# Performance work log

Measured on AMD Instinct MI355X. Metric: run time of the kernel, lower is better.

Reference implementation:

```python
import jax, jax.numpy as jnp
import numpy as np
from jax import lax

N, T, IN, H, HEADS, OUT, E = 20000, 32, 32, 64, 4, 1, 320000


def setup_inputs() -> dict:
    key = jax.random.key(0)
    ks = jax.random.split(key, 18)
    s = 0.1
    inp = {
        "x": jax.random.normal(ks[0], (N, T, IN), jnp.float32),
        "edge_index": jax.random.randint(ks[1], (2, E), 0, N, dtype=jnp.int32),
        # LSTM layer 0 (PyTorch gate order i,f,g,o)
        "l0_Wih": jax.random.normal(ks[2], (4 * H, IN), jnp.float32) * s,
        "l0_Whh": jax.random.normal(ks[3], (4 * H, H), jnp.float32) * s,
        "l0_bih": jax.random.normal(ks[4], (4 * H,), jnp.float32) * s,
        "l0_bhh": jax.random.normal(ks[5], (4 * H,), jnp.float32) * s,
        # LSTM layer 1
        "l1_Wih": jax.random.normal(ks[6], (4 * H, H), jnp.float32) * s,
        "l1_Whh": jax.random.normal(ks[7], (4 * H, H), jnp.float32) * s,
        "l1_bih": jax.random.normal(ks[8], (4 * H,), jnp.float32) * s,
        "l1_bhh": jax.random.normal(ks[9], (4 * H,), jnp.float32) * s,
        # GAT layer 1: in=H, out=H, heads=HEADS (concat)
        "g1_w": jax.random.normal(ks[10], (H, HEADS * H), jnp.float32) * s,
        "g1_as": jax.random.normal(ks[11], (1, HEADS, H), jnp.float32) * s,
        "g1_ad": jax.random.normal(ks[12], (1, HEADS, H), jnp.float32) * s,
        "g1_b": jnp.zeros((HEADS * H,), jnp.float32),
        # GAT layer 2: in=HEADS*H, out=OUT, heads=1
        "g2_w": jax.random.normal(ks[13], (HEADS * H, OUT), jnp.float32) * s,
        "g2_as": jax.random.normal(ks[14], (1, 1, OUT), jnp.float32) * s,
        "g2_ad": jax.random.normal(ks[15], (1, 1, OUT), jnp.float32) * s,
        "g2_b": jnp.zeros((OUT,), jnp.float32),
    }
    return inp


def _lstm_layer(x, Wih, Whh, bih, bhh):
    # x: [N, T, F] -> [N, T, H]
    n = x.shape[0]
    h0 = jnp.zeros((n, Whh.shape[1]), x.dtype)

    def step(carry, xt):
        h, c = carry
        g = xt @ Wih.T + h @ Whh.T + bih + bhh  # [N, 4H]
        i, f, gg, o = jnp.split(g, 4, axis=-1)
        c = jax.nn.sigmoid(f) * c + jax.nn.sigmoid(i) * jnp.tanh(gg)
        h = jax.nn.sigmoid(o) * jnp.tanh(c)
        return (h, c), h

    _, hs = lax.scan(step, (h0, h0), jnp.swapaxes(x, 0, 1))
    return jnp.swapaxes(hs, 0, 1)


def _gat(x, src, dst, n, W, a_src, a_dst, b, heads, outc):
    # PyG GATConv (eval mode, add_self_loops already applied to src/dst)
    xh = (x @ W).reshape(n, heads, outc)              # [N, heads, C]
    al_s = (xh * a_src).sum(-1)                       # [N, heads]
    al_d = (xh * a_dst).sum(-1)
    e = jax.nn.leaky_relu(al_s[src] + al_d[dst], 0.2)  # [E, heads]
    m = jax.ops.segment_max(e, dst, num_segments=n)
    m = jnp.where(jnp.isfinite(m), m, 0.0)
    ex = jnp.exp(e - m[dst])
    den = jax.ops.segment_sum(ex, dst, num_segments=n)
    w = ex / (den[dst] + 1e-16)                       # segment softmax over dst
    out = jax.ops.segment_sum(xh[src] * w[..., None], dst, num_segments=n)
    return out.reshape(n, heads * outc) + b


def reference(x, edge_index, l0_Wih, l0_Whh, l0_bih, l0_bhh, l1_Wih, l1_Whh,
              l1_bih, l1_bhh, g1_w, g1_as, g1_ad, g1_b, g2_w, g2_as, g2_ad, g2_b):
    n = x.shape[0]
    loops = jnp.arange(n, dtype=edge_index.dtype)
    ei = jnp.concatenate([edge_index, jnp.stack([loops, loops])], axis=1)
    src, dst = ei[0], ei[1]
    h = _lstm_layer(x, l0_Wih, l0_Whh, l0_bih, l0_bhh)
    h = _lstm_layer(h, l1_Wih, l1_Whh, l1_bih, l1_bhh)
    h = h[:, -1, :]  # node features from last timestep
    h = jax.nn.relu(_gat(h, src, dst, n, g1_w, g1_as, g1_ad, g1_b, HEADS, H))
    return _gat(h, src, dst, n, g2_w, g2_as, g2_ad, g2_b, 1, OUT)
```

## Files before the change

kernel.cpp:

```cpp
#include <hip/hip_runtime.h>
#include <math.h>

#define NN   20000
#define TT   32
#define INF_ 32
#define HID  64
#define NH   4
#define EE   320000
#define ETOT (EE + NN)
#define ZROW 164
#define NB   80

typedef __attribute__((ext_vector_type(8))) short bf16x8;
typedef __attribute__((ext_vector_type(4))) short short4v;
typedef __attribute__((ext_vector_type(4))) float f32x4;

static __device__ __forceinline__ float lrelu(float x){ return x>0.0f ? x : 0.2f*x; }

static __device__ __forceinline__ unsigned short f2bf(float f){
  unsigned u = __float_as_uint(f);
  unsigned r = u + 0x7fffu + ((u>>16)&1u);
  return (unsigned short)(r>>16);
}
static __device__ __forceinline__ float bf2f(unsigned short h){ return __uint_as_float(((unsigned)h)<<16); }

static __device__ __forceinline__ float lstm_cell(float gi, float gf, float gg, float go, float& c){
  float ef = __expf(-gf), ei = __expf(-gi), eg = __expf(-2.0f*gg);
  float pN = c*(1.0f+ei)*(1.0f+eg) + (1.0f-eg)*(1.0f+ef);
  float pD = (1.0f+ef)*(1.0f+ei)*(1.0f+eg);
  float cc = pN * __builtin_amdgcn_rcpf(pD);
  c = cc;
  float eo = __expf(-go), ec = __expf(-2.0f*cc);
  return (1.0f-ec) * __builtin_amdgcn_rcpf((1.0f+eo)*(1.0f+ec));
}

static __device__ __forceinline__ void edge_sd(const int* __restrict__ ei, int e, int& s, int& d){
  if (e < EE){ s = ei[e]; d = ei[EE + e]; } else { s = e - EE; d = s; }
}

__global__ void kzero_int(int* __restrict__ p, int n){
  int i = blockIdx.x*256 + threadIdx.x;
  if (i < n) p[i] = 0;
}

__global__ void pack_weights(const float* __restrict__ Wih0, const float* __restrict__ Whh0,
                             const float* __restrict__ bih0, const float* __restrict__ bhh0,
                             const float* __restrict__ Wih1, const float* __restrict__ Whh1,
                             const float* __restrict__ bih1, const float* __restrict__ bhh1,
                             unsigned short* __restrict__ Wpk,
                             float* __restrict__ b0, float* __restrict__ b1){
  int idx = blockIdx.x*256 + threadIdx.x;
  if (idx < 49152){
    int fb = idx >> 9;
    int h  = fb & 1;
    int t2 = fb >> 1;
    int ks = t2 % 3, T2 = t2 / 3;
    int T  = T2 & 1, w = T2 >> 1;
    int r  = idx & 511;
    int l  = r >> 3, j = r & 7;
    int pr = l & 15;
    int g  = (pr&3)*64 + w*8 + T*4 + (pr>>2);
    int k  = ks*32 + 4*(l>>4) + (j & 3) + 16*(j >> 2);
    float src = (k < 32) ? Wih0[g*32 + k] : Whh0[g*64 + (k - 32)];
    unsigned short hi = f2bf(src);
    Wpk[idx] = h ? f2bf(src - bf2f(hi)) : hi;
  } else if (idx < 114688){
    int idx2 = idx - 49152;
    int fb = idx2 >> 9;
    int h  = fb & 1;
    int t2 = fb >> 1;
    int ks = t2 & 3, T2 = t2 >> 2;
    int T  = T2 & 1, w = T2 >> 1;
    int r  = idx2 & 511;
    int l  = r >> 3, j = r & 7;
    int pr = l & 15;
    int g  = (pr&3)*64 + w*8 + T*4 + (pr>>2);
    int k  = ks*32 + 4*(l>>4) + (j & 3) + 16*(j >> 2);
    float src = (k < 64) ? Wih1[g*64 + k] : Whh1[g*64 + (k - 64)];
    unsigned short hi = f2bf(src);
    Wpk[idx] = h ? f2bf(src - bf2f(hi)) : hi;
  } else {
    int m = idx - 114688;
    if (m < 256) b0[m] = bih0[m] + bhh0[m];
    else if (m < 512) b1[m-256] = bih1[m-256] + bhh1[m-256];
  }
}

__global__ void count_deg(const int* __restrict__ ei, int* __restrict__ deg){
  int e = blockIdx.x*256 + threadIdx.x;
  if (e >= ETOT) return;
  int s, d; edge_sd(ei, e, s, d);
  atomicAdd(deg + d, 1);
}

__global__ void scan_deg(const int* __restrict__ deg, int* __restrict__ indptr, int* __restrict__ cursor){
  __shared__ int part[256];
  const int t = threadIdx.x;
  const int CH = (NN + 255) / 256;
  const int c0 = t * CH;
  int sum = 0;
  for (int i=0;i<CH;i++){ int idx=c0+i; if (idx<NN) sum += deg[idx]; }
  part[t] = sum; __syncthreads();
  int val = sum;
  for (int off=1; off<256; off<<=1){
    int add = (t>=off) ? part[t-off] : 0;
    __syncthreads();
    val += add; part[t] = val;
    __syncthreads();
  }
  int run = val - sum;
  for (int i=0;i<CH;i++){
    int idx=c0+i;
    if (idx<NN){ indptr[idx]=run; cursor[idx]=run; run += deg[idx]; }
  }
  if (t == 0) indptr[NN] = ETOT;
}

__global__ void scatter_edges(const int* __restrict__ ei, int* __restrict__ cursor, int* __restrict__ csr_src){
  int e = blockIdx.x*256 + threadIdx.x;
  if (e >= ETOT) return;
  int s, d; edge_sd(ei, e, s, d);
  int pos = atomicAdd(cursor + d, 1);
  csr_src[pos] = s;
}

#define PIN_LOAD(dst, p) asm volatile( \
    "global_load_dwordx4 %0, %1, off\n\t" \
    "s_waitcnt vmcnt(0)" \
    : "=&v"(dst) : "v"(p))

__global__ __launch_bounds__(512, 2)
__attribute__((amdgpu_waves_per_eu(2, 2)))
void lstm_mfma(
    const float* __restrict__ x,
    const unsigned short* __restrict__ Wpk,
    const float* __restrict__ b0, const float* __restrict__ b1,
    float* __restrict__ h1out)
{
  __shared__ unsigned short Zh[NB*ZROW];
  __shared__ unsigned short Zl[NB*ZROW];

  const int tid  = threadIdx.x;
  const int lane = tid & 63;
  const int w    = __builtin_amdgcn_readfirstlane(tid >> 6);
  const int ln15 = lane & 15;
  const int lq   = lane >> 4;
  const int gbase = blockIdx.x * NB;

  const bf16x8* wp = (const bf16x8*)Wpk;

  bf16x8 wA0h[2][3], wA0l[2][3], wA1h[2][4], wA1l[2][4];
#pragma unroll
  for (int T=0; T<2; ++T){
#pragma unroll
    for (int ks=0; ks<3; ++ks){
      PIN_LOAD(wA0h[T][ks], wp + (((w*2+T)*3+ks)*2+0)*64 + lane);
      PIN_LOAD(wA0l[T][ks], wp + (((w*2+T)*3+ks)*2+1)*64 + lane);
    }
#pragma unroll
    for (int ks=0; ks<4; ++ks){
      PIN_LOAD(wA1h[T][ks], wp + 6144 + (((w*2+T)*4+ks)*2+0)*64 + lane);
      PIN_LOAD(wA1l[T][ks], wp + 6144 + (((w*2+T)*4+ks)*2+1)*64 + lane);
    }
  }

  f32x4 bv0[2], bv1[2];
#pragma unroll
  for (int T=0; T<2; ++T){
    const int u = w*8 + T*4 + lq;
#pragma unroll
    for (int j=0; j<4; ++j){ bv0[T][j] = b0[j*64+u]; bv1[T][j] = b1[j*64+u]; }
  }

  const int xn1 = tid >> 3,        xk1 = (tid & 7)*4;
  const int xn2 = (512+tid) >> 3,  xk2 = ((512+tid) & 7)*4;
  const float* xp1 = x + (size_t)(gbase + xn1)*(TT*INF_) + xk1;
  const float* xp2 = x + (size_t)(gbase + xn2)*(TT*INF_) + xk2;
  const bool x2 = (tid < 128);

  for (int i = tid; i < NB*ZROW/2; i += 512){ ((unsigned*)Zh)[i] = 0; ((unsigned*)Zl)[i] = 0; }
  __syncthreads();
  {
    float4 v = *(const float4*)xp1;
    unsigned short h_[4], l_[4];
    h_[0]=f2bf(v.x); h_[1]=f2bf(v.y); h_[2]=f2bf(v.z); h_[3]=f2bf(v.w);
    l_[0]=f2bf(v.x-bf2f(h_[0])); l_[1]=f2bf(v.y-bf2f(h_[1]));
    l_[2]=f2bf(v.z-bf2f(h_[2])); l_[3]=f2bf(v.w-bf2f(h_[3]));
    *(uint2*)&Zh[xn1*ZROW + xk1] = make_uint2((unsigned)h_[0]|((unsigned)h_[1]<<16),(unsigned)h_[2]|((unsigned)h_[3]<<16));
    *(uint2*)&Zl[xn1*ZROW + xk1] = make_uint2((unsigned)l_[0]|((unsigned)l_[1]<<16),(unsigned)l_[2]|((unsigned)l_[3]<<16));
    if (x2){
      float4 u = *(const float4*)xp2;
      h_[0]=f2bf(u.x); h_[1]=f2bf(u.y); h_[2]=f2bf(u.z); h_[3]=f2bf(u.w);
      l_[0]=f2bf(u.x-bf2f(h_[0])); l_[1]=f2bf(u.y-bf2f(h_[1]));
      l_[2]=f2bf(u.z-bf2f(h_[2])); l_[3]=f2bf(u.w-bf2f(h_[3]));
      *(uint2*)&Zh[xn2*ZROW + xk2] = make_uint2((unsigned)h_[0]|((unsigned)h_[1]<<16),(unsigned)h_[2]|((unsigned)h_[3]<<16));
      *(uint2*)&Zl[xn2*ZROW + xk2] = make_uint2((unsigned)l_[0]|((unsigned)l_[1]<<16),(unsigned)l_[2]|((unsigned)l_[3]<<16));
    }
  }
  __syncthreads();

  float c0[10], c1[10];
#pragma unroll
  for (int i=0;i<10;i++){ c0[i]=0.f; c1[i]=0.f; }
  f32x4 aL1[2][5];

#define ZFRAG(Zb, node, kz) ({                                            \
    const unsigned short* _p = &Zb[(node)*ZROW + (kz) + 4*lq];            \
    short4v _a = *(const short4v*)_p;                                     \
    short4v _b = *(const short4v*)(_p + 16);                              \
    __builtin_shufflevector(_a, _b, 0,1,2,3,4,5,6,7); })

#define MF(acc, A, B) acc = __builtin_amdgcn_mfma_f32_16x16x32_bf16((A),(B),(acc),0,0,0)

#define HWRITE(hv, col) {                                                 \
    const unsigned short _hh = f2bf(hv);                                  \
    Zh[_n*ZROW + (col)] = _hh;                                            \
    Zl[_n*ZROW + (col)] = f2bf((hv) - bf2f(_hh)); }

  for (int t=0; t<TT; ++t){
    float4 xv1, xv2;
    const bool dox = (t+1 < TT);
    if (dox){ xv1 = *(const float4*)(xp1 + (size_t)(t+1)*INF_);
              if (x2) xv2 = *(const float4*)(xp2 + (size_t)(t+1)*INF_); }

    if (t > 0){
#pragma unroll
      for (int T=0; T<2; ++T){
        const int uc = 96 + w*8 + T*4 + lq;
#pragma unroll
        for (int GG=0; GG<5; ++GG){
          const int _n = GG*16 + ln15;
          float h = lstm_cell(aL1[T][GG][0], aL1[T][GG][1], aL1[T][GG][2], aL1[T][GG][3], c1[T*5+GG]);
          HWRITE(h, uc);
        }
      }
    }

    f32x4 aL0[2][5];
#pragma unroll
    for (int T=0; T<2; ++T)
#pragma unroll
      for (int GG=0; GG<5; ++GG) aL0[T][GG] = bv0[T];

#pragma unroll
    for (int ks=0; ks<3; ++ks){
      const int kz = ks*32;
#pragma unroll
      for (int GG=0; GG<5; ++GG){
        const bf16x8 zh = ZFRAG(Zh, GG*16+ln15, kz);
        const bf16x8 zl = ZFRAG(Zl, GG*16+ln15, kz);
        MF(aL0[0][GG], wA0h[0][ks], zh); MF(aL0[0][GG], wA0h[0][ks], zl); MF(aL0[0][GG], wA0l[0][ks], zh);
        MF(aL0[1][GG], wA0h[1][ks], zh); MF(aL0[1][GG], wA0h[1][ks], zl); MF(aL0[1][GG], wA0l[1][ks], zh);
      }
    }
    __syncthreads();

#pragma unroll
    for (int T=0; T<2; ++T){
      const int uc = 32 + w*8 + T*4 + lq;
#pragma unroll
      for (int GG=0; GG<5; ++GG){
        const int _n = GG*16 + ln15;
        float h = lstm_cell(aL0[T][GG][0], aL0[T][GG][1], aL0[T][GG][2], aL0[T][GG][3], c0[T*5+GG]);
        HWRITE(h, uc);
      }
    }
    if (dox){
      unsigned short h_[4], l_[4];
      h_[0]=f2bf(xv1.x); h_[1]=f2bf(xv1.y); h_[2]=f2bf(xv1.z); h_[3]=f2bf(xv1.w);
      l_[0]=f2bf(xv1.x-bf2f(h_[0])); l_[1]=f2bf(xv1.y-bf2f(h_[1]));
      l_[2]=f2bf(xv1.z-bf2f(h_[2])); l_[3]=f2bf(xv1.w-bf2f(h_[3]));
      *(uint2*)&Zh[xn1*ZROW + xk1] = make_uint2((unsigned)h_[0]|((unsigned)h_[1]<<16),(unsigned)h_[2]|((unsigned)h_[3]<<16));
      *(uint2*)&Zl[xn1*ZROW + xk1] = make_uint2((unsigned)l_[0]|((unsigned)l_[1]<<16),(unsigned)l_[2]|((unsigned)l_[3]<<16));
      if (x2){
        h_[0]=f2bf(xv2.x); h_[1]=f2bf(xv2.y); h_[2]=f2bf(xv2.z); h_[3]=f2bf(xv2.w);
        l_[0]=f2bf(xv2.x-bf2f(h_[0])); l_[1]=f2bf(xv2.y-bf2f(h_[1]));
        l_[2]=f2bf(xv2.z-bf2f(h_[2])); l_[3]=f2bf(xv2.w-bf2f(h_[3]));
        *(uint2*)&Zh[xn2*ZROW + xk2] = make_uint2((unsigned)h_[0]|((unsigned)h_[1]<<16),(unsigned)h_[2]|((unsigned)h_[3]<<16));
        *(uint2*)&Zl[xn2*ZROW + xk2] = make_uint2((unsigned)l_[0]|((unsigned)l_[1]<<16),(unsigned)l_[2]|((unsigned)l_[3]<<16));
      }
    }

#pragma unroll
    for (int T=0; T<2; ++T)
#pragma unroll
      for (int GG=0; GG<5; ++GG) aL1[T][GG] = bv1[T];

#pragma unroll
    for (int ks=2; ks<4; ++ks){
      const int kz = 32 + ks*32;
#pragma unroll
      for (int GG=0; GG<5; ++GG){
        const bf16x8 zh = ZFRAG(Zh, GG*16+ln15, kz);
        const bf16x8 zl = ZFRAG(Zl, GG*16+ln15, kz);
        MF(aL1[0][GG], wA1h[0][ks], zh); MF(aL1[0][GG], wA1h[0][ks], zl); MF(aL1[0][GG], wA1l[0][ks], zh);
        MF(aL1[1][GG], wA1h[1][ks], zh); MF(aL1[1][GG], wA1h[1][ks], zl); MF(aL1[1][GG], wA1l[1][ks], zh);
      }
    }
    __syncthreads();

#pragma unroll
    for (int ks=0; ks<2; ++ks){
      const int kz = 32 + ks*32;
#pragma unroll
      for (int GG=0; GG<5; ++GG){
        const bf16x8 zh = ZFRAG(Zh, GG*16+ln15, kz);
        const bf16x8 zl = ZFRAG(Zl, GG*16+ln15, kz);
        MF(aL1[0][GG], wA1h[0][ks], zh); MF(aL1[0][GG], wA1h[0][ks], zl); MF(aL1[0][GG], wA1l[0][ks], zh);
        MF(aL1[1][GG], wA1h[1][ks], zh); MF(aL1[1][GG], wA1h[1][ks], zl); MF(aL1[1][GG], wA1l[1][ks], zh);
      }
    }
    __syncthreads();
  }

#pragma unroll
  for (int T=0; T<2; ++T){
    const int uc = 96 + w*8 + T*4 + lq;
#pragma unroll
    for (int GG=0; GG<5; ++GG){
      const int _n = GG*16 + ln15;
      float h = lstm_cell(aL1[T][GG][0], aL1[T][GG][1], aL1[T][GG][2], aL1[T][GG][3], c1[T*5+GG]);
      HWRITE(h, uc);
    }
  }
  __syncthreads();

  for (int o = tid; o < NB*64; o += 512){
    const int n = o >> 6, u = o & 63;
    h1out[(size_t)(gbase+n)*64 + u] = bf2f(Zh[n*ZROW + 96 + u]) + bf2f(Zl[n*ZROW + 96 + u]);
  }
#undef ZFRAG
#undef MF
#undef HWRITE
}

__global__ __launch_bounds__(256) void gat1_prep(const float* __restrict__ h1, const float* __restrict__ W,
  const float* __restrict__ as_, const float* __restrict__ ad_,
  float* __restrict__ xh, float* __restrict__ als, float* __restrict__ ald)
{
  __shared__ float hs[8][64];
  const int nb0 = blockIdx.x * 8;
  const int o  = threadIdx.x;
  const int q  = o >> 6, u = o & 63;
  for (int i = o; i < 512; i += 256){
    hs[i>>6][i&63] = h1[(size_t)(nb0 + (i>>6))*64 + (i&63)];
  }
  __syncthreads();
  float acc[8];
#pragma unroll
  for (int nd=0; nd<8; ++nd) acc[nd] = 0.f;
  for (int k=0; k<64; ++k){
    const float wv = W[k*256 + o];
#pragma unroll
    for (int nd=0; nd<8; ++nd) acc[nd] = fmaf(hs[nd][k], wv, acc[nd]);
  }
  const float asv = as_[o], adv = ad_[o];
#pragma unroll
  for (int nd=0; nd<8; ++nd){
    xh[(size_t)(nb0+nd)*256 + o] = acc[nd];
    float ps = acc[nd] * asv;
    float pd = acc[nd] * adv;
#pragma unroll
    for (int off=32; off>=1; off>>=1){ ps += __shfl_xor(ps, off); pd += __shfl_xor(pd, off); }
    if (u == 0){ als[(nb0+nd)*4 + q] = ps; ald[(nb0+nd)*4 + q] = pd; }
  }
}

__global__ __launch_bounds__(256) void gat1_gather(
  const int* __restrict__ indptr, const int* __restrict__ csr_src,
  const float* __restrict__ als, const float* __restrict__ ald,
  const float* __restrict__ xh,  const float* __restrict__ b1g,
  const float* __restrict__ w2,  const float* __restrict__ as2, const float* __restrict__ ad2,
  float* __restrict__ xh2, float* __restrict__ a2s, float* __restrict__ a2d)
{
  const int d = blockIdx.x*4 + (threadIdx.x >> 6);
  const int lane = threadIdx.x & 63;
  if (d >= NN) return;
  const int p0 = indptr[d], p1 = indptr[d+1];

  float aldv[4];
#pragma unroll
  for (int q=0;q<4;q++) aldv[q] = ald[d*4+q];

  float mx[4];
#pragma unroll
  for (int q=0;q<4;q++) mx[q] = -3.4e38f;
  for (int e=p0+lane; e<p1; e+=64){
    int s = csr_src[e];
#pragma unroll
    for (int q=0;q<4;q++){
      float ev = lrelu(als[s*4+q] + aldv[q]);
      mx[q] = fmaxf(mx[q], ev);
    }
  }
#pragma unroll
  for (int off=32; off>=1; off>>=1){
#pragma unroll
    for (int q=0;q<4;q++) mx[q] = fmaxf(mx[q], __shfl_xor(mx[q], off));
  }

  const int q = lane >> 4;
  const float mq = mx[q];
  const float aldq = aldv[q];
  float ax=0.f, ay=0.f, az=0.f, aw=0.f, den=0.f;
  int s_next = (p0 < p1) ? csr_src[p0] : 0;
  for (int e=p0; e<p1; ++e){
    const int s = s_next;
    if (e+1 < p1) s_next = csr_src[e+1];
    float ev = lrelu(als[s*4+q] + aldq);
    float ex = __expf(ev - mq);
    den += ex;
    float4 v = *(const float4*)(xh + (size_t)s*256 + lane*4);
    ax = fmaf(ex, v.x, ax); ay = fmaf(ex, v.y, ay);
    az = fmaf(ex, v.z, az); aw = fmaf(ex, v.w, aw);
  }
  const float rr = 1.0f/(den + 1e-16f);
  const int o = lane*4;
  float v0 = ax*rr + b1g[o+0];
  float v1 = ay*rr + b1g[o+1];
  float v2 = az*rr + b1g[o+2];
  float v3 = aw*rr + b1g[o+3];
  v0 = v0>0.f?v0:0.f; v1 = v1>0.f?v1:0.f; v2 = v2>0.f?v2:0.f; v3 = v3>0.f?v3:0.f;
  float part = v0*w2[o+0] + v1*w2[o+1] + v2*w2[o+2] + v3*w2[o+3];
#pragma unroll
  for (int off=32; off>=1; off>>=1) part += __shfl_xor(part, off);
  if (lane == 0){
    xh2[d] = part;
    a2s[d] = part * as2[0];
    a2d[d] = part * ad2[0];
  }
}

__global__ __launch_bounds__(256) void gat2_gather(
  const int* __restrict__ indptr, const int* __restrict__ csr_src,
  const float* __restrict__ a2s, const float* __restrict__ a2d,
  const float* __restrict__ xh2, const float* __restrict__ b2,
  float* __restrict__ out)
{
  const int d = blockIdx.x*4 + (threadIdx.x >> 6);
  const int lane = threadIdx.x & 63;
  if (d >= NN) return;
  const int p0 = indptr[d], p1 = indptr[d+1];
  const float add = a2d[d];

  float mx = -3.4e38f;
  for (int e=p0+lane; e<p1; e+=64){
    int s = csr_src[e];
    mx = fmaxf(mx, lrelu(a2s[s] + add));
  }
#pragma unroll
  for (int off=32; off>=1; off>>=1) mx = fmaxf(mx, __shfl_xor(mx, off));

  float den = 0.f, num = 0.f;
  for (int e=p0+lane; e<p1; e+=64){
    int s = csr_src[e];
    float ev = lrelu(a2s[s] + add);
    float ex = __expf(ev - mx);
    den += ex;
    num = fmaf(ex, xh2[s], num);
  }
#pragma unroll
  for (int off=32; off>=1; off>>=1){ den += __shfl_xor(den, off); num += __shfl_xor(num, off); }
  if (lane == 0) out[d] = num/(den + 1e-16f) + b2[0];
}

extern "C" void kernel_launch(void* const* d_in, const int* in_sizes, int n_in,
                              void* d_out, int out_size, void* d_ws, size_t ws_size,
                              hipStream_t stream)
{
  const float* x    = (const float*)d_in[0];
  const int*   ei   = (const int*)d_in[1];
  const float* Wih0 = (const float*)d_in[2];
  const float* Whh0 = (const float*)d_in[3];
  const float* bih0 = (const float*)d_in[4];
  const float* bhh0 = (const float*)d_in[5];
  const float* Wih1 = (const float*)d_in[6];
  const float* Whh1 = (const float*)d_in[7];
  const float* bih1 = (const float*)d_in[8];
  const float* bhh1 = (const float*)d_in[9];
  const float* g1w  = (const float*)d_in[10];
  const float* g1as = (const float*)d_in[11];
  const float* g1ad = (const float*)d_in[12];
  const float* g1b  = (const float*)d_in[13];
  const float* g2w  = (const float*)d_in[14];
  const float* g2as = (const float*)d_in[15];
  const float* g2ad = (const float*)d_in[16];
  const float* g2b  = (const float*)d_in[17];

  float* ws  = (float*)d_ws;
  unsigned short* Wpk = (unsigned short*)ws;
  float* b0  = ws + 57344;
  float* b1  = b0 + 256;
  float* h1  = b1 + 256;
  float* xh  = h1 + 1280000;
  float* als = xh + 5120000;
  float* ald = als + 80000;
  float* xh2 = ald + 80000;
  float* a2s = xh2 + 20000;
  float* a2d = a2s + 20000;
  int*   deg    = (int*)(a2d + 20000);
  int*   indptr = deg + 20000;
  int*   cursor = indptr + 20001;
  int*   csr    = cursor + 20000;

  kzero_int<<<(NN+255)/256, 256, 0, stream>>>(deg, NN);
  pack_weights<<<450, 256, 0, stream>>>(Wih0,Whh0,bih0,bhh0,Wih1,Whh1,bih1,bhh1,Wpk,b0,b1);
  count_deg<<<(ETOT+255)/256, 256, 0, stream>>>(ei, deg);
  scan_deg<<<1, 256, 0, stream>>>(deg, indptr, cursor);
  scatter_edges<<<(ETOT+255)/256, 256, 0, stream>>>(ei, cursor, csr);
  lstm_mfma<<<250, 512, 0, stream>>>(x, Wpk, b0, b1, h1);
  gat1_prep<<<NN/8, 256, 0, stream>>>(h1, g1w, g1as, g1ad, xh, als, ald);
  gat1_gather<<<(NN+3)/4, 256, 0, stream>>>(indptr, csr, als, ald, xh, g1b, g2w, g2as, g2ad, xh2, a2s, a2d);
  gat2_gather<<<(NN+3)/4, 256, 0, stream>>>(indptr, csr, a2s, a2d, xh2, g2b, (float*)d_out);
}
```

Before: 421.0 us.

## Split LSTM hidden tiles across 16 waves per block instead of 8

The LSTM kernel now launches 1024 threads per block, and each wave owns one 4-unit gate tile instead of two. Weight fragments, accumulators and cell state per thread are halved, and the weight packing is reindexed to match. This doubles the waves available to hide MFMA and LDS latency within each of the 250 blocks, since the grid underfills the CUs. The cost is heavier __syncthreads among 16 waves and more redundant LDS reads of the shared Z fragments per block.

```diff
diff --git a/kernel.cpp b/kernel.cpp
--- a/kernel.cpp
+++ b/kernel.cpp
@@ -54,12 +54,11 @@
     int fb = idx >> 9;
     int h  = fb & 1;
     int t2 = fb >> 1;
-    int ks = t2 % 3, T2 = t2 / 3;
-    int T  = T2 & 1, w = T2 >> 1;
+    int ks = t2 % 3, tl = t2 / 3;
     int r  = idx & 511;
     int l  = r >> 3, j = r & 7;
     int pr = l & 15;
-    int g  = (pr&3)*64 + w*8 + T*4 + (pr>>2);
+    int g  = (pr&3)*64 + tl*4 + (pr>>2);
     int k  = ks*32 + 4*(l>>4) + (j & 3) + 16*(j >> 2);
     float src = (k < 32) ? Wih0[g*32 + k] : Whh0[g*64 + (k - 32)];
     unsigned short hi = f2bf(src);
@@ -69,12 +68,11 @@
     int fb = idx2 >> 9;
     int h  = fb & 1;
     int t2 = fb >> 1;
-    int ks = t2 & 3, T2 = t2 >> 2;
-    int T  = T2 & 1, w = T2 >> 1;
+    int ks = t2 & 3, tl = t2 >> 2;
     int r  = idx2 & 511;
     int l  = r >> 3, j = r & 7;
     int pr = l & 15;
-    int g  = (pr&3)*64 + w*8 + T*4 + (pr>>2);
+    int g  = (pr&3)*64 + tl*4 + (pr>>2);
     int k  = ks*32 + 4*(l>>4) + (j & 3) + 16*(j >> 2);
     float src = (k < 64) ? Wih1[g*64 + k] : Whh1[g*64 + (k - 64)];
     unsigned short hi = f2bf(src);
@@ -129,8 +127,8 @@
     "s_waitcnt vmcnt(0)" \
     : "=&v"(dst) : "v"(p))
 
-__global__ __launch_bounds__(512, 2)
-__attribute__((amdgpu_waves_per_eu(2, 2)))
+__global__ __launch_bounds__(1024)
+__attribute__((amdgpu_waves_per_eu(4, 4)))
 void lstm_mfma(
     const float* __restrict__ x,
     const unsigned short* __restrict__ Wpk,
@@ -149,60 +147,47 @@
 
   const bf16x8* wp = (const bf16x8*)Wpk;
 
-  bf16x8 wA0h[2][3], wA0l[2][3], wA1h[2][4], wA1l[2][4];
-#pragma unroll
-  for (int T=0; T<2; ++T){
-#pragma unroll
-    for (int ks=0; ks<3; ++ks){
-      PIN_LOAD(wA0h[T][ks], wp + (((w*2+T)*3+ks)*2+0)*64 + lane);
-      PIN_LOAD(wA0l[T][ks], wp + (((w*2+T)*3+ks)*2+1)*64 + lane);
-    }
-#pragma unroll
-    for (int ks=0; ks<4; ++ks){
-      PIN_LOAD(wA1h[T][ks], wp + 6144 + (((w*2+T)*4+ks)*2+0)*64 + lane);
-      PIN_LOAD(wA1l[T][ks], wp + 6144 + (((w*2+T)*4+ks)*2+1)*64 + lane);
-    }
-  }
-
-  f32x4 bv0[2], bv1[2];
-#pragma unroll
-  for (int T=0; T<2; ++T){
-    const int u = w*8 + T*4 + lq;
-#pragma unroll
-    for (int j=0; j<4; ++j){ bv0[T][j] = b0[j*64+u]; bv1[T][j] = b1[j*64+u]; }
-  }
-
-  const int xn1 = tid >> 3,        xk1 = (tid & 7)*4;
-  const int xn2 = (512+tid) >> 3,  xk2 = ((512+tid) & 7)*4;
-  const float* xp1 = x + (size_t)(gbase + xn1)*(TT*INF_) + xk1;
-  const float* xp2 = x + (size_t)(gbase + xn2)*(TT*INF_) + xk2;
-  const bool x2 = (tid < 128);
-
-  for (int i = tid; i < NB*ZROW/2; i += 512){ ((unsigned*)Zh)[i] = 0; ((unsigned*)Zl)[i] = 0; }
+  bf16x8 wA0h[3], wA0l[3], wA1h[4], wA1l[4];
+#pragma unroll
+  for (int ks=0; ks<3; ++ks){
+    PIN_LOAD(wA0h[ks], wp + ((w*3+ks)*2+0)*64 + lane);
+    PIN_LOAD(wA0l[ks], wp + ((w*3+ks)*2+1)*64 + lane);
+  }
+#pragma unroll
+  for (int ks=0; ks<4; ++ks){
+    PIN_LOAD(wA1h[ks], wp + 6144 + ((w*4+ks)*2+0)*64 + lane);
+    PIN_LOAD(wA1l[ks], wp + 6144 + ((w*4+ks)*2+1)*64 + lane);
+  }
+
+  f32x4 bv0, bv1;
+  {
+    const int u = w*4 + lq;
+#pragma unroll
+    for (int j=0; j<4; ++j){ bv0[j] = b0[j*64+u]; bv1[j] = b1[j*64+u]; }
+  }
+
+  const int xn = tid >> 3;
+  const int xk = (tid & 7) * 4;
+  const float* xp = x + (size_t)(gbase + ((xn < NB) ? xn : 0))*(TT*INF_) + xk;
+  const bool xth = (tid < 640);
+
+  for (int i = tid; i < NB*ZROW/2; i += 1024){ ((unsigned*)Zh)[i] = 0; ((unsigned*)Zl)[i] = 0; }
   __syncthreads();
-  {
-    float4 v = *(const float4*)xp1;
+  if (xth){
+    float4 v = *(const float4*)xp;
     unsigned short h_[4], l_[4];
     h_[0]=f2bf(v.x); h_[1]=f2bf(v.y); h_[2]=f2bf(v.z); h_[3]=f2bf(v.w);
     l_[0]=f2bf(v.x-bf2f(h_[0])); l_[1]=f2bf(v.y-bf2f(h_[1]));
     l_[2]=f2bf(v.z-bf2f(h_[2])); l_[3]=f2bf(v.w-bf2f(h_[3]));
-    *(uint2*)&Zh[xn1*ZROW + xk1] = make_uint2((unsigned)h_[0]|((unsigned)h_[1]<<16),(unsigned)h_[2]|((unsigned)h_[3]<<16));
-    *(uint2*)&Zl[xn1*ZROW + xk1] = make_uint2((unsigned)l_[0]|((unsigned)l_[1]<<16),(unsigned)l_[2]|((unsigned)l_[3]<<16));
-    if (x2){
-      float4 u = *(const float4*)xp2;
-      h_[0]=f2bf(u.x); h_[1]=f2bf(u.y); h_[2]=f2bf(u.z); h_[3]=f2bf(u.w);
-      l_[0]=f2bf(u.x-bf2f(h_[0])); l_[1]=f2bf(u.y-bf2f(h_[1]));
-      l_[2]=f2bf(u.z-bf2f(h_[2])); l_[3]=f2bf(u.w-bf2f(h_[3]));
-      *(uint2*)&Zh[xn2*ZROW + xk2] = make_uint2((unsigned)h_[0]|((unsigned)h_[1]<<16),(unsigned)h_[2]|((unsigned)h_[3]<<16));
-      *(uint2*)&Zl[xn2*ZROW + xk2] = make_uint2((unsigned)l_[0]|((unsigned)l_[1]<<16),(unsigned)l_[2]|((unsigned)l_[3]<<16));
-    }
+    *(uint2*)&Zh[xn*ZROW + xk] = make_uint2((unsigned)h_[0]|((unsigned)h_[1]<<16),(unsigned)h_[2]|((unsigned)h_[3]<<16));
+    *(uint2*)&Zl[xn*ZROW + xk] = make_uint2((unsigned)l_[0]|((unsigned)l_[1]<<16),(unsigned)l_[2]|((unsigned)l_[3]<<16));
   }
   __syncthreads();
 
-  float c0[10], c1[10];
-#pragma unroll
-  for (int i=0;i<10;i++){ c0[i]=0.f; c1[i]=0.f; }
-  f32x4 aL1[2][5];
+  float c0[5], c1[5];
+#pragma unroll
+  for (int i=0;i<5;i++){ c0[i]=0.f; c1[i]=0.f; }
+  f32x4 aL1[5];
 
 #define ZFRAG(Zb, node, kz) ({                                            \
     const unsigned short* _p = &Zb[(node)*ZROW + (kz) + 4*lq];            \
@@ -218,29 +203,23 @@
     Zl[_n*ZROW + (col)] = f2bf((hv) - bf2f(_hh)); }
 
   for (int t=0; t<TT; ++t){
-    float4 xv1, xv2;
-    const bool dox = (t+1 < TT);
-    if (dox){ xv1 = *(const float4*)(xp1 + (size_t)(t+1)*INF_);
-              if (x2) xv2 = *(const float4*)(xp2 + (size_t)(t+1)*INF_); }
+    float4 xv;
+    const bool dox = xth && (t+1 < TT);
+    if (dox) xv = *(const float4*)(xp + (size_t)(t+1)*INF_);
 
     if (t > 0){
-#pragma unroll
-      for (int T=0; T<2; ++T){
-        const int uc = 96 + w*8 + T*4 + lq;
-#pragma unroll
-        for (int GG=0; GG<5; ++GG){
-          const int _n = GG*16 + ln15;
-          float h = lstm_cell(aL1[T][GG][0], aL1[T][GG][1], aL1[T][GG][2], aL1[T][GG][3], c1[T*5+GG]);
-          HWRITE(h, uc);
-        }
+      const int uc = 96 + w*4 + lq;
+#pragma unroll
+      for (int GG=0; GG<5; ++GG){
+        const int _n = GG*16 + ln15;
+        float h = lstm_cell(aL1[GG][0], aL1[GG][1], aL1[GG][2], aL1[GG][3], c1[GG]);
+        HWRITE(h, uc);
       }
     }
 
-    f32x4 aL0[2][5];
-#pragma unroll
-    for (int T=0; T<2; ++T)
-#pragma unroll
-      for (int GG=0; GG<5; ++GG) aL0[T][GG] = bv0[T];
+    f32x4 aL0[5];
+#pragma unroll
+    for (int GG=0; GG<5; ++GG) aL0[GG] = bv0;
 
 #pragma unroll
     for (int ks=0; ks<3; ++ks){
@@ -249,42 +228,31 @@
       for (int GG=0; GG<5; ++GG){
         const bf16x8 zh = ZFRAG(Zh, GG*16+ln15, kz);
         const bf16x8 zl = ZFRAG(Zl, GG*16+ln15, kz);
-        MF(aL0[0][GG], wA0h[0][ks], zh); MF(aL0[0][GG], wA0h[0][ks], zl); MF(aL0[0][GG], wA0l[0][ks], zh);
-        MF(aL0[1][GG], wA0h[1][ks], zh); MF(aL0[1][GG], wA0h[1][ks], zl); MF(aL0[1][GG], wA0l[1][ks], zh);
+        MF(aL0[GG], wA0h[ks], zh); MF(aL0[GG], wA0h[ks], zl); MF(aL0[GG], wA0l[ks], zh);
       }
     }
     __syncthreads();
 
-#pragma unroll
-    for (int T=0; T<2; ++T){
-      const int uc = 32 + w*8 + T*4 + lq;
+    {
+      const int uc = 32 + w*4 + lq;
 #pragma unroll
       for (int GG=0; GG<5; ++GG){
         const int _n = GG*16 + ln15;
-        float h = lstm_cell(aL0[T][GG][0], aL0[T][GG][1], aL0[T][GG][2], aL0[T][GG][3], c0[T*5+GG]);
+        float h = lstm_cell(aL0[GG][0], aL0[GG][1], aL0[GG][2], aL0[GG][3], c0[GG]);
         HWRITE(h, uc);
       }
     }
     if (dox){
       unsigned short h_[4], l_[4];
-      h_[0]=f2bf(xv1.x); h_[1]=f2bf(xv1.y); h_[2]=f2bf(xv1.z); h_[3]=f2bf(xv1.w);
-      l_[0]=f2bf(xv1.x-bf2f(h_[0])); l_[1]=f2bf(xv1.y-bf2f(h_[1]));
-      l_[2]=f2bf(xv1.z-bf2f(h_[2])); l_[3]=f2bf(xv1.w-bf2f(h_[3]));
-      *(uint2*)&Zh[xn1*ZROW + xk1] = make_uint2((unsigned)h_[0]|((unsigned)h_[1]<<16),(unsigned)h_[2]|((unsigned)h_[3]<<16));
-      *(uint2*)&Zl[xn1*ZROW + xk1] = make_uint2((unsigned)l_[0]|((unsigned)l_[1]<<16),(unsigned)l_[2]|((unsigned)l_[3]<<16));
-      if (x2){
-        h_[0]=f2bf(xv2.x); h_[1]=f2bf(xv2.y); h_[2]=f2bf(xv2.z); h_[3]=f2bf(xv2.w);
-        l_[0]=f2bf(xv2.x-bf2f(h_[0])); l_[1]=f2bf(xv2.y-bf2f(h_[1]));
-        l_[2]=f2bf(xv2.z-bf2f(h_[2])); l_[3]=f2bf(xv2.w-bf2f(h_[3]));
-        *(uint2*)&Zh[xn2*ZROW + xk2] = make_uint2((unsigned)h_[0]|((unsigned)h_[1]<<16),(unsigned)h_[2]|((unsigned)h_[3]<<16));
-        *(uint2*)&Zl[xn2*ZROW + xk2] = make_uint2((unsigned)l_[0]|((unsigned)l_[1]<<16),(unsigned)l_[2]|((unsigned)l_[3]<<16));
-      }
-    }
-
-#pragma unroll
-    for (int T=0; T<2; ++T)
-#pragma unroll
-      for (int GG=0; GG<5; ++GG) aL1[T][GG] = bv1[T];
+      h_[0]=f2bf(xv.x); h_[1]=f2bf(xv.y); h_[2]=f2bf(xv.z); h_[3]=f2bf(xv.w);
+      l_[0]=f2bf(xv.x-bf2f(h_[0])); l_[1]=f2bf(xv.y-bf2f(h_[1]));
+      l_[2]=f2bf(xv.z-bf2f(h_[2])); l_[3]=f2bf(xv.w-bf2f(h_[3]));
+      *(uint2*)&Zh[xn*ZROW + xk] = make_uint2((unsigned)h_[0]|((unsigned)h_[1]<<16),(unsigned)h_[2]|((unsigned)h_[3]<<16));
+      *(uint2*)&Zl[xn*ZROW + xk] = make_uint2((unsigned)l_[0]|((unsigned)l_[1]<<16),(unsigned)l_[2]|((unsigned)l_[3]<<16));
+    }
+
+#pragma unroll
+    for (int GG=0; GG<5; ++GG) aL1[GG] = bv1;
 
 #pragma unroll
     for (int ks=2; ks<4; ++ks){
@@ -293,8 +261,7 @@
       for (int GG=0; GG<5; ++GG){
         const bf16x8 zh = ZFRAG(Zh, GG*16+ln15, kz);
         const bf16x8 zl = ZFRAG(Zl, GG*16+ln15, kz);
-        MF(aL1[0][GG], wA1h[0][ks], zh); MF(aL1[0][GG], wA1h[0][ks], zl); MF(aL1[0][GG], wA1l[0][ks], zh);
-        MF(aL1[1][GG], wA1h[1][ks], zh); MF(aL1[1][GG], wA1h[1][ks], zl); MF(aL1[1][GG], wA1l[1][ks], zh);
+        MF(aL1[GG], wA1h[ks], zh); MF(aL1[GG], wA1h[ks], zl); MF(aL1[GG], wA1l[ks], zh);
       }
     }
     __syncthreads();
@@ -306,26 +273,24 @@
       for (int GG=0; GG<5; ++GG){
         const bf16x8 zh = ZFRAG(Zh, GG*16+ln15, kz);
         const bf16x8 zl = ZFRAG(Zl, GG*16+ln15, kz);
-        MF(aL1[0][GG], wA1h[0][ks], zh); MF(aL1[0][GG], wA1h[0][ks], zl); MF(aL1[0][GG], wA1l[0][ks], zh);
-        MF(aL1[1][GG], wA1h[1][ks], zh); MF(aL1[1][GG], wA1h[1][ks], zl); MF(aL1[1][GG], wA1l[1][ks], zh);
+        MF(aL1[GG], wA1h[ks], zh); MF(aL1[GG], wA1h[ks], zl); MF(aL1[GG], wA1l[ks], zh);
       }
     }
     __syncthreads();
   }
 
-#pragma unroll
-  for (int T=0; T<2; ++T){
-    const int uc = 96 + w*8 + T*4 + lq;
+  {
+    const int uc = 96 + w*4 + lq;
 #pragma unroll
     for (int GG=0; GG<5; ++GG){
       const int _n = GG*16 + ln15;
-      float h = lstm_cell(aL1[T][GG][0], aL1[T][GG][1], aL1[T][GG][2], aL1[T][GG][3], c1[T*5+GG]);
+      float h = lstm_cell(aL1[GG][0], aL1[GG][1], aL1[GG][2], aL1[GG][3], c1[GG]);
       HWRITE(h, uc);
     }
   }
   __syncthreads();
 
-  for (int o = tid; o < NB*64; o += 512){
+  for (int o = tid; o < NB*64; o += 1024){
     const int n = o >> 6, u = o & 63;
     h1out[(size_t)(gbase+n)*64 + u] = bf2f(Zh[n*ZROW + 96 + u]) + bf2f(Zl[n*ZROW + 96 + u]);
   }
@@ -508,7 +473,7 @@
   count_deg<<<(ETOT+255)/256, 256, 0, stream>>>(ei, deg);
   scan_deg<<<1, 256, 0, stream>>>(deg, indptr, cursor);
   scatter_edges<<<(ETOT+255)/256, 256, 0, stream>>>(ei, cursor, csr);
-  lstm_mfma<<<250, 512, 0, stream>>>(x, Wpk, b0, b1, h1);
+  lstm_mfma<<<250, 1024, 0, stream>>>(x, Wpk, b0, b1, h1);
   gat1_prep<<<NN/8, 256, 0, stream>>>(h1, g1w, g1as, g1ad, xh, als, ald);
   gat1_gather<<<(NN+3)/4, 256, 0, stream>>>(indptr, csr, als, ald, xh, g1b, g2w, g2as, g2ad, xh2, a2s, a2d);
   gat2_gather<<<(NN+3)/4, 256, 0, stream>>>(indptr, csr, a2s, a2d, xh2, g2b, (float*)d_out);
```

Result: no change. 412.9 us (-1.9%).
